# Performance work log

Hardware: AMD Instinct MI355X
Metric: run time of the kernel (lower is better)

Reference implementation:

```python
import jax, jax.numpy as jnp
import numpy as np

B, T, C, H, W = 4, 5, 64, 48, 48
F = 10                      # num_feat
N = T * H * W               # 11520, ffnn1 is Linear(N, N)


def setup_inputs() -> dict:
    key = jax.random.key(0)
    ks = jax.random.split(key, 9)
    sc = lambda *shape: 1.0 / np.sqrt(shape[-1])
    return {
        "input": jax.random.normal(ks[0], (B, T, C, H, W), jnp.float32),
        "input1": jax.random.normal(ks[1], (1,), jnp.float32),
        "act_weights": jax.random.uniform(ks[2], (3,), jnp.float32),
        # conv1: Conv1d(C, F, 1) -> weight [F, C] (kernel dim squeezed), bias [F]
        "conv1_w": jax.random.normal(ks[3], (F, C), jnp.float32) * sc(F, C),
        "conv1_b": jax.random.normal(ks[4], (F,), jnp.float32) * 0.01,
        # G3: Conv1d(C, F, 1)
        "g3_w": jax.random.normal(ks[5], (F, C), jnp.float32) * sc(F, C),
        "g3_b": jax.random.normal(ks[6], (F,), jnp.float32) * 0.01,
        # ffnn1: Linear(N, N)
        "ffnn_w": jax.random.normal(ks[7], (N, N), jnp.float32) * sc(N, N),
        "ffnn_b": jax.random.normal(ks[8], (N,), jnp.float32) * 0.01,
    }


def reference(input, input1, act_weights, conv1_w, conv1_b, g3_w, g3_b, ffnn_w, ffnn_b):
    b, t, c, h, w = input.shape
    n = t * h * w
    # [B, C, N]: transpose(1,2) then flatten T,H,W
    x = jnp.transpose(input, (0, 2, 1, 3, 4)).reshape(b, c, n)

    # conv1 (1x1) -> [B, F, N]; AvgPool1d(F) over the feat dim -> [B, N]
    c1 = jnp.einsum('bcn,fc->bfn', x, conv1_w) + conv1_b[None, :, None]
    s = jnp.mean(c1, axis=1)                      # [B, N]

    # ffnn1 (same Linear used in all three branches in the original)
    z = s @ ffnn_w.T + ffnn_b                     # [B, N]

    # G3 projection -> [B, N, F]
    g3 = jnp.einsum('bcn,fc->bnf', x, g3_w) + g3_b[None, None, :]

    # diag_embed(z) @ g3^T is exactly a per-position scale of g3 by z.
    gate = (act_weights[0] * jax.nn.relu(z)
            + act_weights[1] * jax.nn.sigmoid(z)
            + act_weights[2] * jax.nn.softmax(z, axis=1))  # [B, N]
    out = gate[:, :, None] * g3                   # [B, N, F]

    out = out.reshape(b, t, h, w, g3.shape[-1])   # [B, T, H, W, F]
    return jnp.transpose(out, (0, 1, 4, 2, 3))    # [B, T, F, H, W]
```

## Files before the change

kernel.cpp:

```cpp
#include <hip/hip_runtime.h>
#include <math.h>

#define Bsz 4
#define Tsz 5
#define Csz 64
#define Fsz 10
#define Hsz 48
#define Wsz 48
#define HWsz (Hsz*Wsz)
#define Nsz (Tsz*HWsz)
#define N4  (Nsz/4)
#define KC4 576
#define NCHUNK 5

typedef float float4n __attribute__((ext_vector_type(4)));

#define O_S   0
#define O_G3  (O_S + Bsz*Nsz)
#define O_Z   (O_G3 + Bsz*Fsz*Nsz)
#define O_MX  (O_Z + Bsz*Nsz)
#define O_SM  (O_MX + 4)

__global__ __launch_bounds__(256) void k_sg3(const float* __restrict__ in,
                                             const float* __restrict__ cw,
                                             const float* __restrict__ cb,
                                             const float* __restrict__ g3w,
                                             const float* __restrict__ g3b,
                                             float* __restrict__ ws) {
    __shared__ float sw[Fsz*Csz];
    __shared__ float scw[Csz + 1];
    if (threadIdx.x < Csz) {
        float a = 0.f;
        #pragma unroll
        for (int f = 0; f < Fsz; ++f) a += cw[f*Csz + threadIdx.x];
        scw[threadIdx.x] = a * (1.0f/Fsz);
    }
    if (threadIdx.x == 0) {
        float a = 0.f;
        #pragma unroll
        for (int f = 0; f < Fsz; ++f) a += cb[f];
        scw[Csz] = a * (1.0f/Fsz);
    }
    for (int i = threadIdx.x; i < Fsz*Csz; i += 256) sw[i] = g3w[i];
    __syncthreads();

    const int n = blockIdx.x * 256 + threadIdx.x;
    const int b = blockIdx.y;
    const int t = n / HWsz;
    const int p = n - t * HWsz;

    const float* xp = in + ((size_t)(b*Tsz + t) * Csz) * HWsz + p;

    float accs = 0.f;
    float accf[Fsz];
    #pragma unroll
    for (int f = 0; f < Fsz; ++f) accf[f] = 0.f;

    for (int c = 0; c < Csz; ++c) {
        float xv = xp[(size_t)c * HWsz];
        accs = fmaf(xv, scw[c], accs);
        #pragma unroll
        for (int f = 0; f < Fsz; ++f) accf[f] = fmaf(xv, sw[f*Csz + c], accf[f]);
    }

    float* s   = ws + O_S;
    float* g3t = ws + O_G3;
    s[b*Nsz + n] = accs + scw[Csz];
    #pragma unroll
    for (int f = 0; f < Fsz; ++f)
        g3t[((size_t)b*Fsz + f) * Nsz + n] = accf[f] + g3b[f];
}

#define DOT4(ACC, WV, SV) \
    ACC = fmaf(WV.x, SV.x, ACC); ACC = fmaf(WV.y, SV.y, ACC); \
    ACC = fmaf(WV.z, SV.z, ACC); ACC = fmaf(WV.w, SV.w, ACC)

__global__ __launch_bounds__(256) void k_gemv(const float* __restrict__ Wm,
                                              const float* __restrict__ fb,
                                              float* __restrict__ ws) {
    __shared__ float4 slds[Bsz][KC4];
    const int tid  = threadIdx.x;
    const int wave = tid >> 6;
    const int lane = tid & 63;
    const int row0 = blockIdx.x * 16 + wave * 4;

    const float4n* w0 = (const float4n*)(Wm + (size_t)(row0    ) * Nsz);
    const float4n* w1 = (const float4n*)(Wm + (size_t)(row0 + 1) * Nsz);
    const float4n* w2 = (const float4n*)(Wm + (size_t)(row0 + 2) * Nsz);
    const float4n* w3 = (const float4n*)(Wm + (size_t)(row0 + 3) * Nsz);
    const float4* s4 = (const float4*)(ws + O_S);

    float acc[4][4];
    #pragma unroll
    for (int r = 0; r < 4; ++r)
        #pragma unroll
        for (int b = 0; b < 4; ++b) acc[r][b] = 0.f;

    for (int ch = 0; ch < NCHUNK; ++ch) {
        const int c0 = ch * KC4;
        __syncthreads();
        #pragma unroll
        for (int k = 0; k < (Bsz*KC4)/256; ++k) {
            const int q = k*256 + tid;
            const int b = q / KC4;
            const int j = q - b * KC4;
            slds[b][j] = s4[(size_t)b * N4 + c0 + j];
        }
        __syncthreads();

        #pragma unroll
        for (int jj = 0; jj < KC4/64; ++jj) {
            const int j  = jj*64 + lane;
            const int n4 = c0 + j;
            const float4n a0 = __builtin_nontemporal_load(w0 + n4);
            const float4n a1 = __builtin_nontemporal_load(w1 + n4);
            const float4n a2 = __builtin_nontemporal_load(w2 + n4);
            const float4n a3 = __builtin_nontemporal_load(w3 + n4);
            float4 sv;
            sv = slds[0][j];
            DOT4(acc[0][0], a0, sv); DOT4(acc[1][0], a1, sv);
            DOT4(acc[2][0], a2, sv); DOT4(acc[3][0], a3, sv);
            sv = slds[1][j];
            DOT4(acc[0][1], a0, sv); DOT4(acc[1][1], a1, sv);
            DOT4(acc[2][1], a2, sv); DOT4(acc[3][1], a3, sv);
            sv = slds[2][j];
            DOT4(acc[0][2], a0, sv); DOT4(acc[1][2], a1, sv);
            DOT4(acc[2][2], a2, sv); DOT4(acc[3][2], a3, sv);
            sv = slds[3][j];
            DOT4(acc[0][3], a0, sv); DOT4(acc[1][3], a1, sv);
            DOT4(acc[2][3], a2, sv); DOT4(acc[3][3], a3, sv);
        }
    }

    #pragma unroll
    for (int r = 0; r < 4; ++r)
        #pragma unroll
        for (int b = 0; b < 4; ++b)
            #pragma unroll
            for (int off = 32; off > 0; off >>= 1)
                acc[r][b] += __shfl_xor(acc[r][b], off, 64);

    if (lane == 0) {
        float* z = ws + O_Z;
        #pragma unroll
        for (int r = 0; r < 4; ++r) {
            const float bias = fb[row0 + r];
            #pragma unroll
            for (int b = 0; b < 4; ++b)
                z[(size_t)b*Nsz + row0 + r] = acc[r][b] + bias;
        }
    }
}

__global__ __launch_bounds__(256) void k_stats(float* __restrict__ ws) {
    const int b = blockIdx.x;
    const float* zb = (const float*)ws + O_Z + (size_t)b * Nsz;
    const int lane = threadIdx.x & 63;
    const int wave = threadIdx.x >> 6;
    __shared__ float red[4];
    __shared__ float bcast;

    float m = -INFINITY;
    for (int i = threadIdx.x; i < Nsz; i += 256) m = fmaxf(m, zb[i]);
    #pragma unroll
    for (int off = 32; off > 0; off >>= 1) m = fmaxf(m, __shfl_xor(m, off, 64));
    if (lane == 0) red[wave] = m;
    __syncthreads();
    if (threadIdx.x == 0)
        bcast = fmaxf(fmaxf(red[0], red[1]), fmaxf(red[2], red[3]));
    __syncthreads();
    m = bcast;

    float sum = 0.f;
    for (int i = threadIdx.x; i < Nsz; i += 256) sum += expf(zb[i] - m);
    #pragma unroll
    for (int off = 32; off > 0; off >>= 1) sum += __shfl_xor(sum, off, 64);
    if (lane == 0) red[wave] = sum;
    __syncthreads();
    if (threadIdx.x == 0) {
        ws[O_MX + b] = m;
        ws[O_SM + b] = red[0] + red[1] + red[2] + red[3];
    }
}

__global__ __launch_bounds__(256) void k_out(const float* __restrict__ aw,
                                             const float* __restrict__ ws,
                                             float* __restrict__ out) {
    const int n = blockIdx.x * 256 + threadIdx.x;
    const int b = blockIdx.y;

    const float zv  = ws[O_Z + (size_t)b*Nsz + n];
    const float a0 = aw[0], a1 = aw[1], a2 = aw[2];
    const float mxb = ws[O_MX + b];
    const float smb = ws[O_SM + b];

    const float gate = a0 * fmaxf(zv, 0.f)
                     + a1 / (1.f + expf(-zv))
                     + a2 * expf(zv - mxb) / smb;

    const int t = n / HWsz;
    const int p = n - t * HWsz;
    const float* gp = ws + O_G3 + (size_t)b * Fsz * Nsz + n;
    float* ob = out + ((size_t)(b*Tsz + t) * Fsz) * HWsz + p;
    #pragma unroll
    for (int f = 0; f < Fsz; ++f)
        ob[(size_t)f * HWsz] = gate * gp[(size_t)f * Nsz];
}

extern "C" void kernel_launch(void* const* d_in, const int* in_sizes, int n_in,
                              void* d_out, int out_size, void* d_ws, size_t ws_size,
                              hipStream_t stream) {
    const float* input  = (const float*)d_in[0];
    const float* aw     = (const float*)d_in[2];
    const float* conv1w = (const float*)d_in[3];
    const float* conv1b = (const float*)d_in[4];
    const float* g3w    = (const float*)d_in[5];
    const float* g3b    = (const float*)d_in[6];
    const float* ffnw   = (const float*)d_in[7];
    const float* ffnb   = (const float*)d_in[8];
    float* out = (float*)d_out;
    float* ws  = (float*)d_ws;

    k_sg3  <<<dim3(Nsz/256, Bsz), 256, 0, stream>>>(input, conv1w, conv1b, g3w, g3b, ws);
    k_gemv <<<Nsz/16, 256, 0, stream>>>(ffnw, ffnb, ws);
    k_stats<<<Bsz, 256, 0, stream>>>(ws);
    k_out  <<<dim3(Nsz/256, Bsz), 256, 0, stream>>>(aw, ws, out);
}
```

Baseline: 686.2 us.

## Interleave s by batch and read it directly from global in GEMV

The s vector is now stored interleaved as [N][B] so each position's four batch values are contiguous. The GEMV drops its LDS staging, chunking and block barriers and reads s straight from global (L2/cache) as float4s alongside the weight stream. This removes the syncthreads stalls and LDS traffic, at the cost of more global/cache load instructions per weight element.

```diff
diff --git a/kernel.cpp b/kernel.cpp
--- a/kernel.cpp
+++ b/kernel.cpp
@@ -10,8 +10,6 @@
 #define HWsz (Hsz*Wsz)
 #define Nsz (Tsz*HWsz)
 #define N4  (Nsz/4)
-#define KC4 576
-#define NCHUNK 5
 
 typedef float float4n __attribute__((ext_vector_type(4)));
 
@@ -63,32 +61,26 @@
         for (int f = 0; f < Fsz; ++f) accf[f] = fmaf(xv, sw[f*Csz + c], accf[f]);
     }
 
-    float* s   = ws + O_S;
+    float* st  = ws + O_S;
     float* g3t = ws + O_G3;
-    s[b*Nsz + n] = accs + scw[Csz];
+    st[n*4 + b] = accs + scw[Csz];
     #pragma unroll
     for (int f = 0; f < Fsz; ++f)
         g3t[((size_t)b*Fsz + f) * Nsz + n] = accf[f] + g3b[f];
 }
-
-#define DOT4(ACC, WV, SV) \
-    ACC = fmaf(WV.x, SV.x, ACC); ACC = fmaf(WV.y, SV.y, ACC); \
-    ACC = fmaf(WV.z, SV.z, ACC); ACC = fmaf(WV.w, SV.w, ACC)
 
 __global__ __launch_bounds__(256) void k_gemv(const float* __restrict__ Wm,
                                               const float* __restrict__ fb,
                                               float* __restrict__ ws) {
-    __shared__ float4 slds[Bsz][KC4];
-    const int tid  = threadIdx.x;
-    const int wave = tid >> 6;
-    const int lane = tid & 63;
+    const int wave = threadIdx.x >> 6;
+    const int lane = threadIdx.x & 63;
     const int row0 = blockIdx.x * 16 + wave * 4;
 
     const float4n* w0 = (const float4n*)(Wm + (size_t)(row0    ) * Nsz);
     const float4n* w1 = (const float4n*)(Wm + (size_t)(row0 + 1) * Nsz);
     const float4n* w2 = (const float4n*)(Wm + (size_t)(row0 + 2) * Nsz);
     const float4n* w3 = (const float4n*)(Wm + (size_t)(row0 + 3) * Nsz);
-    const float4* s4 = (const float4*)(ws + O_S);
+    const float4n* st = (const float4n*)(ws + O_S);
 
     float acc[4][4];
     #pragma unroll
@@ -96,39 +88,26 @@
         #pragma unroll
         for (int b = 0; b < 4; ++b) acc[r][b] = 0.f;
 
-    for (int ch = 0; ch < NCHUNK; ++ch) {
-        const int c0 = ch * KC4;
-        __syncthreads();
-        #pragma unroll
-        for (int k = 0; k < (Bsz*KC4)/256; ++k) {
-            const int q = k*256 + tid;
-            const int b = q / KC4;
-            const int j = q - b * KC4;
-            slds[b][j] = s4[(size_t)b * N4 + c0 + j];
-        }
-        __syncthreads();
-
-        #pragma unroll
-        for (int jj = 0; jj < KC4/64; ++jj) {
-            const int j  = jj*64 + lane;
-            const int n4 = c0 + j;
-            const float4n a0 = __builtin_nontemporal_load(w0 + n4);
-            const float4n a1 = __builtin_nontemporal_load(w1 + n4);
-            const float4n a2 = __builtin_nontemporal_load(w2 + n4);
-            const float4n a3 = __builtin_nontemporal_load(w3 + n4);
-            float4 sv;
-            sv = slds[0][j];
-            DOT4(acc[0][0], a0, sv); DOT4(acc[1][0], a1, sv);
-            DOT4(acc[2][0], a2, sv); DOT4(acc[3][0], a3, sv);
-            sv = slds[1][j];
-            DOT4(acc[0][1], a0, sv); DOT4(acc[1][1], a1, sv);
-            DOT4(acc[2][1], a2, sv); DOT4(acc[3][1], a3, sv);
-            sv = slds[2][j];
-            DOT4(acc[0][2], a0, sv); DOT4(acc[1][2], a1, sv);
-            DOT4(acc[2][2], a2, sv); DOT4(acc[3][2], a3, sv);
-            sv = slds[3][j];
-            DOT4(acc[0][3], a0, sv); DOT4(acc[1][3], a1, sv);
-            DOT4(acc[2][3], a2, sv); DOT4(acc[3][3], a3, sv);
+    for (int it = 0; it < N4/64; ++it) {
+        const int j = it*64 + lane;
+        const float4n a0 = __builtin_nontemporal_load(w0 + j);
+        const float4n a1 = __builtin_nontemporal_load(w1 + j);
+        const float4n a2 = __builtin_nontemporal_load(w2 + j);
+        const float4n a3 = __builtin_nontemporal_load(w3 + j);
+        const float4n s0 = st[4*j + 0];
+        const float4n s1 = st[4*j + 1];
+        const float4n s2 = st[4*j + 2];
+        const float4n s3 = st[4*j + 3];
+        #pragma unroll
+        for (int b = 0; b < 4; ++b) {
+            acc[0][b] = fmaf(a0.x, s0[b], acc[0][b]); acc[0][b] = fmaf(a0.y, s1[b], acc[0][b]);
+            acc[0][b] = fmaf(a0.z, s2[b], acc[0][b]); acc[0][b] = fmaf(a0.w, s3[b], acc[0][b]);
+            acc[1][b] = fmaf(a1.x, s0[b], acc[1][b]); acc[1][b] = fmaf(a1.y, s1[b], acc[1][b]);
+            acc[1][b] = fmaf(a1.z, s2[b], acc[1][b]); acc[1][b] = fmaf(a1.w, s3[b], acc[1][b]);
+            acc[2][b] = fmaf(a2.x, s0[b], acc[2][b]); acc[2][b] = fmaf(a2.y, s1[b], acc[2][b]);
+            acc[2][b] = fmaf(a2.z, s2[b], acc[2][b]); acc[2][b] = fmaf(a2.w, s3[b], acc[2][b]);
+            acc[3][b] = fmaf(a3.x, s0[b], acc[3][b]); acc[3][b] = fmaf(a3.y, s1[b], acc[3][b]);
+            acc[3][b] = fmaf(a3.z, s2[b], acc[3][b]); acc[3][b] = fmaf(a3.w, s3[b], acc[3][b]);
         }
     }
 
```

After: 703.3 us. +2.5%, slower.
